# Kernel tuning notes

Measured on AMD Instinct MI355X. Metric: run time of the kernel, lower is better.

Reference implementation:

```python
import jax, jax.numpy as jnp
import numpy as np

B, P, ENC, DEC, ATT, EMB, V, CAPLEN = 128, 196, 2048, 512, 512, 300, 10000, 51


def setup_inputs() -> dict:
    key = jax.random.key(0)
    ks = jax.random.split(key, 20)
    s = 0.02
    lens = jax.random.randint(ks[2], (B, 1), 2, CAPLEN + 1)
    lens = lens.at[0, 0].set(CAPLEN)  # ensure max decode length == CAPLEN-1 (static T)
    return {
        'encoder_out': jax.random.normal(ks[0], (B, P, ENC), jnp.float32),
        'encoded_captions': jax.random.randint(ks[1], (B, CAPLEN), 0, V),
        'caption_lengths': lens,
        'W_enc_att': jax.random.normal(ks[3], (ATT, ENC)) * s,
        'b_enc_att': jnp.zeros((ATT,)),
        'W_dec_att': jax.random.normal(ks[4], (ATT, DEC)) * s,
        'b_dec_att': jnp.zeros((ATT,)),
        'w_full_att': jax.random.normal(ks[5], (ATT,)) * s,
        'b_full_att': jnp.zeros(()),
        'embedding': jax.random.uniform(ks[6], (V, EMB), minval=-0.1, maxval=0.1),
        'W_ih': jax.random.normal(ks[7], (4 * DEC, EMB + ENC)) * s,
        'b_ih': jnp.zeros((4 * DEC,)),
        'W_hh': jax.random.normal(ks[8], (4 * DEC, DEC)) * s,
        'b_hh': jnp.zeros((4 * DEC,)),
        'W_init_h': jax.random.normal(ks[9], (DEC, ENC)) * s,
        'b_init_h': jnp.zeros((DEC,)),
        'W_init_c': jax.random.normal(ks[10], (DEC, ENC)) * s,
        'b_init_c': jnp.zeros((DEC,)),
        'W_fbeta': jax.random.normal(ks[11], (ENC, DEC)) * s,
        'b_fbeta': jnp.zeros((ENC,)),
        'W_fc': jax.random.uniform(ks[12], (V, DEC), minval=-0.1, maxval=0.1),
        'b_fc': jnp.zeros((V,)),
    }


def reference(encoder_out, encoded_captions, caption_lengths,
              W_enc_att, b_enc_att, W_dec_att, b_dec_att, w_full_att, b_full_att,
              embedding, W_ih, b_ih, W_hh, b_hh,
              W_init_h, b_init_h, W_init_c, b_init_c,
              W_fbeta, b_fbeta, W_fc, b_fc):
    lens = caption_lengths[:, 0]
    sort_ind = jnp.argsort(-lens)                      # descending length sort
    lens_s = lens[sort_ind]
    enc = encoder_out[sort_ind]                        # [B,P,ENC]
    caps = encoded_captions[sort_ind]                  # [B,CAPLEN]
    emb = embedding[caps]                              # [B,CAPLEN,EMB]
    mean_enc = enc.mean(axis=1)
    h0 = mean_enc @ W_init_h.T + b_init_h
    c0 = mean_enc @ W_init_c.T + b_init_c
    att1 = enc @ W_enc_att.T + b_enc_att               # precomputed [B,P,ATT]
    decode_lengths = lens_s - 1
    T = caps.shape[1] - 1                              # static max decode length
    mask = jnp.arange(T)[:, None] < decode_lengths[None, :]   # [T,B]
    emb_t = jnp.transpose(emb[:, :T, :], (1, 0, 2))    # [T,B,EMB]

    def step(carry, xs):
        h, c = carry
        e_t, m_t = xs
        att2 = h @ W_dec_att.T + b_dec_att             # [B,ATT]
        score = jnp.einsum('bpa,a->bp', jax.nn.relu(att1 + att2[:, None, :]), w_full_att) + b_full_att
        alpha = jax.nn.softmax(score, axis=1)          # [B,P]
        awe = jnp.einsum('bp,bpe->be', alpha, enc)     # [B,ENC]
        gate = jax.nn.sigmoid(h @ W_fbeta.T + b_fbeta)
        awe = gate * awe
        x = jnp.concatenate([e_t, awe], axis=1)        # [B,EMB+ENC]
        gates = x @ W_ih.T + b_ih + h @ W_hh.T + b_hh
        i, f, g, o = jnp.split(gates, 4, axis=1)
        i, f, o = jax.nn.sigmoid(i), jax.nn.sigmoid(f), jax.nn.sigmoid(o)
        g = jnp.tanh(g)
        c_new = f * c + i * g
        h_new = o * jnp.tanh(c_new)
        m = m_t[:, None]
        # state only advances for still-active (length > t) rows
        h2 = jnp.where(m, h_new, h)
        c2 = jnp.where(m, c_new, c)
        preds = h_new @ W_fc.T + b_fc                  # dropout is identity in eval
        preds = jnp.where(m, preds, 0.0)
        alpha = jnp.where(m, alpha, 0.0)
        return (h2, c2), (preds, alpha)

    (_, _), (preds, alphas) = jax.lax.scan(step, (h0, c0), (emb_t, mask))
    predictions = jnp.transpose(preds, (1, 0, 2))      # [B,T,V]
    alphas = jnp.transpose(alphas, (1, 0, 2))          # [B,T,P]
    return predictions, caps, decode_lengths, alphas, sort_ind
```

## Files before the change

kernel.cpp:

```cpp
#include <hip/hip_runtime.h>
#include <math.h>

#define B 128
#define PP 196
#define ENC 2048
#define DEC 512
#define ATTD 512
#define EMB 300
#define VV 10000
#define CAPLEN 51
#define TT 50
#define KPAD 2880
#define NPPAD 10112

static const long long OFF_PRED = 0LL;
static const long long OFF_CAPS = 64000000LL;
static const long long OFF_DECL = 64006528LL;
static const long long OFF_ALPH = 64006656LL;
static const long long OFF_SORT = 65261056LL;

typedef unsigned short ushort_t;
typedef unsigned int uint_t;
typedef short bf8 __attribute__((ext_vector_type(8)));
typedef float f4 __attribute__((ext_vector_type(4)));

__device__ __forceinline__ float sigf(float x){ return 1.f/(1.f+expf(-x)); }
__device__ __forceinline__ float b2f(ushort_t u){
  union{uint_t i; float f;} v; v.i = ((uint_t)u)<<16; return v.f;
}
__device__ __forceinline__ ushort_t f2b(float f){
  union{float f; uint_t i;} v; v.f = f;
  uint_t r = v.i + 0x7fffu + ((v.i>>16)&1u);
  return (ushort_t)(r>>16);
}
__device__ __forceinline__ uint_t pack2(float lo, float hi){
  return (uint_t)f2b(lo) | ((uint_t)f2b(hi)<<16);
}
__device__ __forceinline__ float2 b2x2(uint_t u){
  union{uint_t i; float f;} a,b; a.i = u<<16; b.i = u & 0xffff0000u;
  return make_float2(a.f, b.f);
}

__device__ __forceinline__ void gemm128x64(
    const ushort_t* __restrict__ Ab, int lda, int m0,
    const ushort_t* __restrict__ Bb, int ldb, int n0,
    int Kbeg, int Kend, int mbound,
    ushort_t* As, ushort_t* Bs, int tid, f4 acc[4][2])
{
  const int r = tid>>2, cby = (tid&3)*8;
  const int w = tid>>6, l = tid&63;
  const int wm = w>>1, wn = w&1, lr = l&15, lk = (l>>4)*8;
  for (int k0=Kbeg; k0<Kend; k0+=32){
    uint4 qa0 = *(const uint4*)(Ab + (size_t)(m0+r)*lda    + k0 + cby);
    uint4 qa1 = *(const uint4*)(Ab + (size_t)(m0+64+r)*lda + k0 + cby);
    uint4 qb  = *(const uint4*)(Bb + (size_t)(n0+r)*ldb    + k0 + cby);
    __syncthreads();
    *(uint4*)(As + r*40      + cby) = qa0;
    *(uint4*)(As + (64+r)*40 + cby) = qa1;
    *(uint4*)(Bs + r*40      + cby) = qb;
    __syncthreads();
    bf8 b0 = *(const bf8*)(Bs + (wn*32+lr)*40    + lk);
    bf8 b1 = *(const bf8*)(Bs + (wn*32+16+lr)*40 + lk);
    #pragma unroll
    for (int fm=0; fm<4; fm++){
      if (wm*64 + fm*16 >= mbound) break;
      bf8 a = *(const bf8*)(As + (wm*64+fm*16+lr)*40 + lk);
      acc[fm][0] = __builtin_amdgcn_mfma_f32_16x16x32_bf16(a, b0, acc[fm][0], 0, 0, 0);
      acc[fm][1] = __builtin_amdgcn_mfma_f32_16x16x32_bf16(a, b1, acc[fm][1], 0, 0, 0);
    }
  }
}

__global__ __launch_bounds__(128) void k_prep(const int* __restrict__ cap_len,
    const int* __restrict__ enc_caps, float* __restrict__ out,
    int* __restrict__ sort_i, int* __restrict__ decl_i, int* __restrict__ caps_i,
    int* __restrict__ nact_d){
  __shared__ int lens[B];
  __shared__ int sind[B];
  __shared__ int s_dl[B];
  int t = threadIdx.x;
  lens[t] = cap_len[t];
  __syncthreads();
  int my = lens[t];
  int rank = 0;
  for (int j=0;j<B;j++){
    int lj = lens[j];
    if (lj > my || (lj == my && j < t)) rank++;
  }
  sind[rank] = t;
  __syncthreads();
  int src = sind[t];
  sort_i[t] = src;
  int dl = lens[src]-1;
  decl_i[t] = dl;
  s_dl[t] = dl;
  out[OFF_DECL+t] = (float)dl;
  out[OFF_SORT+t] = (float)src;
  for (int j=0;j<CAPLEN;j++){
    int v = enc_caps[src*CAPLEN+j];
    caps_i[t*CAPLEN+j] = v;
    out[OFF_CAPS + t*CAPLEN + j] = (float)v;
  }
  __syncthreads();
  if (t < TT){
    int cnt = 0;
    for (int b2=0;b2<B;b2++) cnt += (s_dl[b2] > t) ? 1 : 0;
    nact_d[t] = cnt;
  }
}

__global__ __launch_bounds__(256) void k_mean(const float* __restrict__ enc,
    const int* __restrict__ sort_i, float* __restrict__ meanb){
  int b = blockIdx.x;
  int e = blockIdx.y*256 + threadIdx.x;
  int sb = sort_i[b];
  const float* p0 = enc + (size_t)sb*PP*ENC + e;
  float s = 0.f;
  for (int p=0;p<PP;p++) s += p0[(size_t)p*ENC];
  meanb[b*ENC+e] = s * (1.0f/PP);
}

__global__ __launch_bounds__(256) void k_init(const float* __restrict__ meanb,
    const float* __restrict__ Wh, const float* __restrict__ bh,
    const float* __restrict__ Wc, const float* __restrict__ bc,
    float* __restrict__ h, float* __restrict__ c, ushort_t* __restrict__ xb_s){
  __shared__ float aT[64*132];
  __shared__ float wT[64*36];
  int tid = threadIdx.x;
  int n0 = blockIdx.x*32;
  const float* Wm  = blockIdx.y ? Wc : Wh;
  const float* bia = blockIdx.y ? bc : bh;
  float* dst = blockIdx.y ? c : h;
  int bt = tid&15, nt = tid>>4;
  float acc[8][2] = {};
  for (int k0=0;k0<ENC;k0+=64){
    for (int idx=tid; idx<64*128; idx+=256){
      int k=idx&63, m=idx>>6;
      aT[k*132+m] = meanb[m*ENC + k0+k];
    }
    for (int idx=tid; idx<64*32; idx+=256){
      int k=idx&63, n=idx>>6;
      wT[k*36+n] = Wm[(size_t)(n0+n)*ENC + k0+k];
    }
    __syncthreads();
    #pragma unroll 4
    for (int k=0;k<64;k++){
      float a[8], wv[2];
      *(float4*)&a[0] = *(const float4*)&aT[k*132+bt*8];
      *(float4*)&a[4] = *(const float4*)&aT[k*132+bt*8+4];
      *(float2*)&wv[0] = *(const float2*)&wT[k*36+nt*2];
      #pragma unroll
      for (int i=0;i<8;i++){ acc[i][0]+=a[i]*wv[0]; acc[i][1]+=a[i]*wv[1]; }
    }
    __syncthreads();
  }
  #pragma unroll
  for (int i=0;i<8;i++){
    int m = bt*8+i;
    #pragma unroll
    for (int j=0;j<2;j++){
      int n = n0+nt*2+j;
      float v = acc[i][j] + bia[n];
      dst[m*DEC+n] = v;
      if (blockIdx.y == 0) xb_s[(size_t)m*KPAD + n] = f2b(v);
    }
  }
}

__global__ __launch_bounds__(256) void k_wkb(const float* __restrict__ Whh,
    const float* __restrict__ Wih, uint_t* __restrict__ wkb_u){
  int n = blockIdx.x;
  uint_t* dst = wkb_u + (size_t)n*(KPAD/2);
  for (int u=threadIdx.x; u<KPAD/2; u+=256){
    int k = 2*u; float a, bvl;
    if (k < 512){ float2 v = *(const float2*)(Whh + (size_t)n*512 + k); a=v.x; bvl=v.y; }
    else if (k < 2860){ float2 v = *(const float2*)(Wih + (size_t)n*2348 + (k-512)); a=v.x; bvl=v.y; }
    else { a=0.f; bvl=0.f; }
    dst[u] = pack2(a, bvl);
  }
}
__global__ __launch_bounds__(256) void k_wcatb(const float* __restrict__ Wda,
    const float* __restrict__ Wfb, uint_t* __restrict__ wcat_u){
  int n = blockIdx.x;
  const float* src = (n < 512) ? (Wda + (size_t)n*512) : (Wfb + (size_t)(n-512)*512);
  uint_t* dst = wcat_u + (size_t)n*256;
  int u = threadIdx.x;
  float2 v = *(const float2*)(src + 2*u);
  dst[u] = pack2(v.x, v.y);
}
__global__ __launch_bounds__(256) void k_wfcb(const float* __restrict__ Wfc,
    uint_t* __restrict__ wfc_u){
  int n = blockIdx.x;
  uint_t* dst = wfc_u + (size_t)n*256;
  int u = threadIdx.x;
  if (n < VV){
    float2 v = *(const float2*)(Wfc + (size_t)n*512 + 2*u);
    dst[u] = pack2(v.x, v.y);
  } else dst[u] = 0u;
}
__global__ __launch_bounds__(256) void k_weab(const float* __restrict__ Wea,
    uint_t* __restrict__ wea_u){
  int n = blockIdx.x;
  uint_t* dst = wea_u + (size_t)n*1024;
  for (int u=threadIdx.x; u<1024; u+=256){
    float2 v = *(const float2*)(Wea + (size_t)n*2048 + 2*u);
    dst[u] = pack2(v.x, v.y);
  }
}
__global__ __launch_bounds__(160) void k_embb(const float* __restrict__ embedding,
    const int* __restrict__ caps_i, uint_t* __restrict__ embb_u){
  int b = blockIdx.x, t = blockIdx.y, tid = threadIdx.x;
  if (tid >= 150) return;
  int tok = caps_i[b*CAPLEN+t];
  float2 v = *(const float2*)(embedding + (size_t)tok*EMB + 2*tid);
  embb_u[((size_t)b*TT+t)*150 + tid] = pack2(v.x, v.y);
}
__global__ __launch_bounds__(256) void k_xpad(uint_t* __restrict__ xb_u){
  for (int u=threadIdx.x; u<1280; u+=256){
    int r = u/10, cu = u - r*10;
    xb_u[(size_t)r*(KPAD/2) + 1430 + cu] = 0u;
  }
}
__global__ __launch_bounds__(256) void k_encb(const float* __restrict__ enc,
    const int* __restrict__ sort_i, ushort_t* __restrict__ encb){
  int row = blockIdx.x;
  int b = row/PP, p = row - b*PP;
  int sb = sort_i[b];
  const float4* s4 = (const float4*)(enc + ((size_t)sb*PP+p)*ENC);
  uint4* d4 = (uint4*)(encb + (size_t)row*ENC);
  int tid = threadIdx.x;
  float4 f0 = s4[tid*2], f1 = s4[tid*2+1];
  uint4 q;
  q.x = pack2(f0.x,f0.y); q.y = pack2(f0.z,f0.w);
  q.z = pack2(f1.x,f1.y); q.w = pack2(f1.z,f1.w);
  d4[tid] = q;
}

__global__ __launch_bounds__(256) void k_zero(const int* __restrict__ decl_i,
    float* __restrict__ out){
  int blk = blockIdx.x;
  int b = blk/TT, t = blk - b*TT;
  if (t < decl_i[b]) return;
  float4 z = {0.f,0.f,0.f,0.f};
  float4* p = (float4*)(out + OFF_PRED + ((size_t)b*TT+t)*VV);
  for (int i=threadIdx.x; i<VV/4; i+=256) p[i] = z;
  size_t ao = (size_t)OFF_ALPH + ((size_t)b*TT+t)*PP;
  if (threadIdx.x < PP) out[ao + threadIdx.x] = 0.f;
}

__global__ __launch_bounds__(256) void k_att1g(const ushort_t* __restrict__ encb,
    const ushort_t* __restrict__ weab, const float* __restrict__ bea,
    ushort_t* __restrict__ attb){
  __shared__ ushort_t As[128*40];
  __shared__ ushort_t Bs[64*40];
  int tid = threadIdx.x;
  int m0 = blockIdx.x*128, n0 = blockIdx.y*64;
  f4 acc[4][2] = {};
  gemm128x64(encb, 2048, m0, weab, 2048, n0, 0, 2048, 128, As, Bs, tid, acc);
  int w = tid>>6, l = tid&63, wm = w>>1, wn = w&1;
  #pragma unroll
  for (int fm=0; fm<4; fm++)
    #pragma unroll
    for (int fn=0; fn<2; fn++)
      #pragma unroll
      for (int rr=0; rr<4; rr++){
        int m = m0 + wm*64 + fm*16 + (l>>4)*4 + rr;
        int n = n0 + wn*32 + fn*16 + (l&15);
        attb[(size_t)m*ATTD + n] = f2b(acc[fm][fn][rr] + bea[n]);
      }
}

__global__ __launch_bounds__(256) void k_att1_f32(const float* __restrict__ enc,
    const float* __restrict__ Wea, const float* __restrict__ bea,
    const int* __restrict__ sort_i, ushort_t* __restrict__ attb){
  __shared__ float aT[64*132];
  __shared__ float wT[64*68];
  int tid = threadIdx.x;
  int m0 = blockIdx.x*128;
  int n0 = blockIdx.y*64;
  int bt = tid&15, nt = tid>>4;
  float acc[8][4] = {};
  for (int k0=0;k0<ENC;k0+=64){
    for (int idx=tid; idx<64*128; idx+=256){
      int k=idx&63, m=idx>>6;
      int mg = m0+m;
      int b = mg/PP; int p = mg - b*PP;
      int sb = sort_i[b];
      aT[k*132+m] = enc[((size_t)sb*PP + p)*ENC + k0+k];
    }
    for (int idx=tid; idx<64*64; idx+=256){
      int k=idx&63, n=idx>>6;
      wT[k*68+n] = Wea[(size_t)(n0+n)*ENC + k0+k];
    }
    __syncthreads();
    #pragma unroll 4
    for (int k=0;k<64;k++){
      float a[8], wv[4];
      *(float4*)&a[0] = *(const float4*)&aT[k*132+bt*8];
      *(float4*)&a[4] = *(const float4*)&aT[k*132+bt*8+4];
      *(float4*)&wv[0] = *(const float4*)&wT[k*68+nt*4];
      #pragma unroll
      for (int i=0;i<8;i++)
        #pragma unroll
        for (int j=0;j<4;j++) acc[i][j] += a[i]*wv[j];
    }
    __syncthreads();
  }
  #pragma unroll
  for (int i=0;i<8;i++){
    int mg = m0+bt*8+i;
    #pragma unroll
    for (int j=0;j<4;j++){
      int n = n0+nt*4+j;
      attb[(size_t)mg*ATTD + n] = f2b(acc[i][j] + bea[n]);
    }
  }
}

__global__ __launch_bounds__(256) void k_hmats(const ushort_t* __restrict__ xb,
    const ushort_t* __restrict__ wcatb, const float* __restrict__ bda,
    const float* __restrict__ bfb, const int* __restrict__ nact_d,
    float* __restrict__ att2s, float* __restrict__ gate, int t){
  __shared__ ushort_t As[128*40];
  __shared__ ushort_t Bs[64*40];
  int tid = threadIdx.x;
  int n0 = blockIdx.x*64;
  int mb = nact_d[t];
  f4 acc[4][2] = {};
  gemm128x64(xb, KPAD, 0, wcatb, 512, n0, 0, 512, mb, As, Bs, tid, acc);
  int w = tid>>6, l = tid&63, wm = w>>1, wn = w&1;
  #pragma unroll
  for (int fm=0; fm<4; fm++)
    #pragma unroll
    for (int fn=0; fn<2; fn++)
      #pragma unroll
      for (int rr=0; rr<4; rr++){
        int m = wm*64 + fm*16 + (l>>4)*4 + rr;
        int n = n0 + wn*32 + fn*16 + (l&15);
        float v = acc[fm][fn][rr];
        if (n < 512) att2s[m*512+n] = v + bda[n];
        else         gate[m*2048 + (n-512)] = sigf(v + bfb[n-512]);
      }
}

template<bool FULLT>
__global__ __launch_bounds__(512) void k_score(const ushort_t* __restrict__ attb,
    const float* __restrict__ att2s, const float* __restrict__ wfa,
    const float* __restrict__ bfa, const int* __restrict__ decl_i,
    float* __restrict__ alb, float* __restrict__ out,
    uint_t* __restrict__ xb_u, const uint_t* __restrict__ embb_u,
    const float* __restrict__ embedding, const int* __restrict__ caps_i, int t){
  int b = blockIdx.x, tid = threadIdx.x;
  if (t >= decl_i[b]) return;
  __shared__ float s_a2[512], s_w[512], s_sc[200], s_red[8], s_red2[8];
  if (FULLT){
    if (tid < 150) xb_u[b*(KPAD/2) + 256 + tid] = embb_u[((size_t)b*TT+t)*150 + tid];
  } else {
    if (tid < 150){
      int tok = caps_i[b*CAPLEN+t];
      float2 e = *(const float2*)(embedding + (size_t)tok*EMB + 2*tid);
      xb_u[b*(KPAD/2) + 256 + tid] = pack2(e.x, e.y);
    }
  }
  s_a2[tid] = att2s[b*512+tid];
  s_w[tid]  = wfa[tid];
  __syncthreads();
  int wid = tid>>6, lane = tid&63;
  float b0 = bfa[0];
  for (int p=wid; p<PP; p+=8){
    uint4 q = ((const uint4*)(attb + ((size_t)b*PP + p)*ATTD))[lane];
    int j = lane*8;
    float2 x0=b2x2(q.x), x1=b2x2(q.y), x2=b2x2(q.z), x3=b2x2(q.w);
    float s = fmaxf(x0.x+s_a2[j+0],0.f)*s_w[j+0] + fmaxf(x0.y+s_a2[j+1],0.f)*s_w[j+1]
            + fmaxf(x1.x+s_a2[j+2],0.f)*s_w[j+2] + fmaxf(x1.y+s_a2[j+3],0.f)*s_w[j+3]
            + fmaxf(x2.x+s_a2[j+4],0.f)*s_w[j+4] + fmaxf(x2.y+s_a2[j+5],0.f)*s_w[j+5]
            + fmaxf(x3.x+s_a2[j+6],0.f)*s_w[j+6] + fmaxf(x3.y+s_a2[j+7],0.f)*s_w[j+7];
    #pragma unroll
    for (int off=32;off;off>>=1) s += __shfl_down(s,off);
    if (lane==0) s_sc[p] = s + b0;
  }
  __syncthreads();
  float sc = (tid<PP) ? s_sc[tid] : -1e30f;
  float mx = sc;
  #pragma unroll
  for (int off=32;off;off>>=1) mx = fmaxf(mx, __shfl_down(mx,off));
  if (lane==0) s_red[wid] = mx;
  __syncthreads();
  mx = s_red[0];
  #pragma unroll
  for (int i=1;i<8;i++) mx = fmaxf(mx, s_red[i]);
  float e = (tid<PP) ? expf(sc-mx) : 0.f;
  float sm = e;
  #pragma unroll
  for (int off=32;off;off>>=1) sm += __shfl_down(sm,off);
  if (lane==0) s_red2[wid] = sm;
  __syncthreads();
  float tot = 0.f;
  #pragma unroll
  for (int i=0;i<8;i++) tot += s_red2[i];
  float inv = 1.f/tot;
  if (tid<PP){
    float al = e*inv;
    alb[b*PP+tid] = al;
    out[(size_t)OFF_ALPH + ((size_t)b*TT+t)*PP + tid] = al;
  }
}

template<bool ENCB_>
__global__ __launch_bounds__(256) void k_awe(const ushort_t* __restrict__ encb,
    const float* __restrict__ enc, const int* __restrict__ sort_i,
    const float* __restrict__ alb, const float* __restrict__ gate,
    const int* __restrict__ decl_i, uint_t* __restrict__ xb_u, int t){
  int b = blockIdx.x, seg = blockIdx.y, tid = threadIdx.x;
  if (t >= decl_i[b]) return;
  __shared__ float s_al[PP];
  if (tid < PP) s_al[tid] = alb[b*PP+tid];
  __syncthreads();
  int ch = seg*512 + tid*2;
  float a0=0.f, a1=0.f;
  if (ENCB_){
    const uint_t* E = (const uint_t*)encb + (size_t)b*PP*(ENC/2) + (ch>>1);
    #pragma unroll 4
    for (int p=0;p<PP;p++){
      float2 u = b2x2(E[(size_t)p*(ENC/2)]);
      float al = s_al[p];
      a0 += al*u.x; a1 += al*u.y;
    }
  } else {
    const float2* E = (const float2*)(enc + (size_t)sort_i[b]*PP*ENC + ch);
    #pragma unroll 4
    for (int p=0;p<PP;p++){
      float2 u = E[(size_t)p*(ENC/2)];
      float al = s_al[p];
      a0 += al*u.x; a1 += al*u.y;
    }
  }
  float g0 = gate[b*ENC+ch], g1 = gate[b*ENC+ch+1];
  xb_u[b*(KPAD/2) + 406 + seg*256 + tid] = pack2(a0*g0, a1*g1);
}

__global__ __launch_bounds__(256) void k_b1g(const ushort_t* __restrict__ xb,
    const ushort_t* __restrict__ wkb, const int* __restrict__ nact_d,
    float* __restrict__ pbuf, int t){
  __shared__ ushort_t As[128*40];
  __shared__ ushort_t Bs[64*40];
  int tid = threadIdx.x;
  int n0 = blockIdx.x*64;
  int s  = blockIdx.y;
  int Kb = s*736, Ke = min(KPAD, Kb+736);
  int mb = nact_d[t];
  f4 acc[4][2] = {};
  gemm128x64(xb, KPAD, 0, wkb, KPAD, n0, Kb, Ke, mb, As, Bs, tid, acc);
  int w = tid>>6, l = tid&63, wm = w>>1, wn = w&1;
  #pragma unroll
  for (int fm=0; fm<4; fm++)
    #pragma unroll
    for (int fn=0; fn<2; fn++)
      #pragma unroll
      for (int rr=0; rr<4; rr++){
        int m = wm*64 + fm*16 + (l>>4)*4 + rr;
        int n = n0 + wn*32 + fn*16 + (l&15);
        pbuf[((size_t)s*B + m)*2048 + n] = acc[fm][fn][rr];
      }
}

__global__ __launch_bounds__(256) void k_b2(const float* __restrict__ pbuf,
    const float* __restrict__ b_ih, const float* __restrict__ b_hh,
    const int* __restrict__ decl_i, float* __restrict__ h, float* __restrict__ c,
    ushort_t* __restrict__ hnb, ushort_t* __restrict__ xb_s, int t){
  int b = blockIdx.x;
  int j = blockIdx.y*256 + threadIdx.x;
  float gi = b_ih[j]        + b_hh[j];
  float gf = b_ih[512+j]    + b_hh[512+j];
  float gg = b_ih[1024+j]   + b_hh[1024+j];
  float go = b_ih[1536+j]   + b_hh[1536+j];
  #pragma unroll
  for (int s=0;s<4;s++){
    const float* p = pbuf + ((size_t)s*B + b)*2048;
    gi += p[j]; gf += p[512+j]; gg += p[1024+j]; go += p[1536+j];
  }
  float hold = h[b*DEC+j];
  float cn = sigf(gf)*c[b*DEC+j] + sigf(gi)*tanhf(gg);
  float hn = sigf(go)*tanhf(cn);
  bool act = t < decl_i[b];
  if (act){ h[b*DEC+j] = hn; c[b*DEC+j] = cn; }
  hnb[b*DEC+j] = f2b(hn);
  xb_s[(size_t)b*KPAD + j] = f2b(act ? hn : hold);
}

__global__ __launch_bounds__(256) void k_predg(const ushort_t* __restrict__ hnb,
    const ushort_t* __restrict__ wfcb, const float* __restrict__ b_fc,
    const int* __restrict__ nact_d, float* __restrict__ out, int t){
  __shared__ ushort_t As[128*40];
  __shared__ ushort_t Bs[64*40];
  int tid = threadIdx.x;
  int n0 = blockIdx.x*64;
  int mb = nact_d[t];
  f4 acc[4][2] = {};
  gemm128x64(hnb, 512, 0, wfcb, 512, n0, 0, 512, mb, As, Bs, tid, acc);
  int w = tid>>6, l = tid&63, wm = w>>1, wn = w&1;
  #pragma unroll
  for (int fm=0; fm<4; fm++)
    #pragma unroll
    for (int fn=0; fn<2; fn++)
      #pragma unroll
      for (int rr=0; rr<4; rr++){
        int m = wm*64 + fm*16 + (l>>4)*4 + rr;
        int n = n0 + wn*32 + fn*16 + (l&15);
        if (m < mb && n < VV)
          out[OFF_PRED + ((size_t)m*TT + t)*VV + n] = acc[fm][fn][rr] + b_fc[n];
      }
}

extern "C" void kernel_launch(void* const* d_in, const int* in_sizes, int n_in,
                              void* d_out, int out_size, void* d_ws, size_t ws_size,
                              hipStream_t stream){
  const float* enc       = (const float*)d_in[0];
  const int*   caps_in   = (const int*)d_in[1];
  const int*   caplen    = (const int*)d_in[2];
  const float* W_enc_att = (const float*)d_in[3];
  const float* b_enc_att = (const float*)d_in[4];
  const float* W_dec_att = (const float*)d_in[5];
  const float* b_dec_att = (const float*)d_in[6];
  const float* w_full_att= (const float*)d_in[7];
  const float* b_full_att= (const float*)d_in[8];
  const float* embedding = (const float*)d_in[9];
  const float* W_ih      = (const float*)d_in[10];
  const float* b_ih      = (const float*)d_in[11];
  const float* W_hh      = (const float*)d_in[12];
  const float* b_hh      = (const float*)d_in[13];
  const float* W_init_h  = (const float*)d_in[14];
  const float* b_init_h  = (const float*)d_in[15];
  const float* W_init_c  = (const float*)d_in[16];
  const float* b_init_c  = (const float*)d_in[17];
  const float* W_fbeta   = (const float*)d_in[18];
  const float* b_fbeta   = (const float*)d_in[19];
  const float* W_fc      = (const float*)d_in[20];
  const float* b_fc      = (const float*)d_in[21];
  float* out = (float*)d_out;

  float* W = (float*)d_ws;
  size_t o = 0;
  auto A = [&](size_t n){ float* p = W + o; o += n; return p; };

  bool FULL = ws_size >= 168000000ull;

  float* h      = A(65536);
  float* c      = A(65536);
  float* att2s  = A(65536);
  float* gate   = A(262144);
  float* alb    = A(25088);
  float* meanb  = A(262144);
  float* pbuf   = A(1048576);
  ushort_t* xb   = (ushort_t*)A(184320);
  ushort_t* wkb  = (ushort_t*)A(2949120);
  ushort_t* wcatb= (ushort_t*)A(655360);
  ushort_t* wfcb = (ushort_t*)A(2588672);
  ushort_t* hnb  = (ushort_t*)A(32768);
  ushort_t* attb = (ushort_t*)A(6422528);
  int* ip = (int*)A(6848);
  int* sort_i = ip;
  int* decl_i = ip + 128;
  int* nact_d = ip + 256;
  int* caps_i = ip + 320;
  ushort_t* weab = nullptr;
  uint_t*   embb_u = nullptr;
  ushort_t* encb = nullptr;
  if (FULL){
    weab   = (ushort_t*)A(524288);
    embb_u = (uint_t*)A(960000);
    encb   = (ushort_t*)A(25690112);
  }
  uint_t* xb_u = (uint_t*)xb;

  k_prep<<<1,128,0,stream>>>(caplen, caps_in, out, sort_i, decl_i, caps_i, nact_d);
  k_mean<<<dim3(128,8),256,0,stream>>>(enc, sort_i, meanb);
  k_init<<<dim3(16,2),256,0,stream>>>(meanb, W_init_h, b_init_h, W_init_c, b_init_c, h, c, xb);
  k_wkb<<<2048,256,0,stream>>>(W_hh, W_ih, (uint_t*)wkb);
  k_wcatb<<<2560,256,0,stream>>>(W_dec_att, W_fbeta, (uint_t*)wcatb);
  k_wfcb<<<NPPAD,256,0,stream>>>(W_fc, (uint_t*)wfcb);
  k_xpad<<<1,256,0,stream>>>(xb_u);
  k_zero<<<6400,256,0,stream>>>(decl_i, out);
  if (FULL){
    k_weab<<<512,256,0,stream>>>(W_enc_att, (uint_t*)weab);
    k_embb<<<dim3(128,50),160,0,stream>>>(embedding, caps_i, embb_u);
    k_encb<<<25088,256,0,stream>>>(enc, sort_i, encb);
    k_att1g<<<dim3(196,8),256,0,stream>>>(encb, weab, b_enc_att, attb);
  } else {
    k_att1_f32<<<dim3(196,8),256,0,stream>>>(enc, W_enc_att, b_enc_att, sort_i, attb);
  }

  for (int t=0;t<TT;t++){
    k_hmats<<<40,256,0,stream>>>(xb, wcatb, b_dec_att, b_fbeta, nact_d, att2s, gate, t);
    if (FULL)
      k_score<true><<<128,512,0,stream>>>(attb, att2s, w_full_att, b_full_att, decl_i,
          alb, out, xb_u, embb_u, embedding, caps_i, t);
    else
      k_score<false><<<128,512,0,stream>>>(attb, att2s, w_full_att, b_full_att, decl_i,
          alb, out, xb_u, embb_u, embedding, caps_i, t);
    if (FULL)
      k_awe<true><<<dim3(128,4),256,0,stream>>>(encb, enc, sort_i, alb, gate, decl_i, xb_u, t);
    else
      k_awe<false><<<dim3(128,4),256,0,stream>>>(encb, enc, sort_i, alb, gate, decl_i, xb_u, t);
    k_b1g<<<dim3(32,4),256,0,stream>>>(xb, wkb, nact_d, pbuf, t);
    k_b2<<<dim3(128,2),256,0,stream>>>(pbuf, b_ih, b_hh, decl_i, h, c, hnb, xb, t);
    k_predg<<<158,256,0,stream>>>(hnb, wfcb, b_fc, nact_d, out, t);
  }
}
```

Measured before the change: 4.724 ms.

## Fuse score with attention-weighted sum, fuse LSTM GEMM with cell update, batch FC

Merges the attention softmax and the attention-weighted encoder sum into one kernel, and merges the LSTM gate GEMM with the cell update. This drops the split-K partial buffer and the per-step b2 kernel; interleaving the gate weight rows lets each block hold i/f/g/o for the same hidden units. The vocabulary projection moves out of the time loop into one batched launch over all steps, using stored hidden states. The shared GEMM helper also gains register prefetch of the next K tile. In exchange, the gate GEMM now runs the full K on only 32 blocks with no split-K, and the awe part runs on 128 blocks instead of 512.

```diff
diff --git a/kernel.cpp b/kernel.cpp
--- a/kernel.cpp
+++ b/kernel.cpp
@@ -50,23 +50,29 @@
   const int r = tid>>2, cby = (tid&3)*8;
   const int w = tid>>6, l = tid&63;
   const int wm = w>>1, wn = w&1, lr = l&15, lk = (l>>4)*8;
+  uint4 qa0 = *(const uint4*)(Ab + (size_t)(m0+r)*lda    + Kbeg + cby);
+  uint4 qa1 = *(const uint4*)(Ab + (size_t)(m0+64+r)*lda + Kbeg + cby);
+  uint4 qb  = *(const uint4*)(Bb + (size_t)(n0+r)*ldb    + Kbeg + cby);
   for (int k0=Kbeg; k0<Kend; k0+=32){
-    uint4 qa0 = *(const uint4*)(Ab + (size_t)(m0+r)*lda    + k0 + cby);
-    uint4 qa1 = *(const uint4*)(Ab + (size_t)(m0+64+r)*lda + k0 + cby);
-    uint4 qb  = *(const uint4*)(Bb + (size_t)(n0+r)*ldb    + k0 + cby);
     __syncthreads();
     *(uint4*)(As + r*40      + cby) = qa0;
     *(uint4*)(As + (64+r)*40 + cby) = qa1;
     *(uint4*)(Bs + r*40      + cby) = qb;
     __syncthreads();
+    if (k0+32 < Kend){
+      qa0 = *(const uint4*)(Ab + (size_t)(m0+r)*lda    + k0+32 + cby);
+      qa1 = *(const uint4*)(Ab + (size_t)(m0+64+r)*lda + k0+32 + cby);
+      qb  = *(const uint4*)(Bb + (size_t)(n0+r)*ldb    + k0+32 + cby);
+    }
     bf8 b0 = *(const bf8*)(Bs + (wn*32+lr)*40    + lk);
     bf8 b1 = *(const bf8*)(Bs + (wn*32+16+lr)*40 + lk);
     #pragma unroll
     for (int fm=0; fm<4; fm++){
-      if (wm*64 + fm*16 >= mbound) break;
-      bf8 a = *(const bf8*)(As + (wm*64+fm*16+lr)*40 + lk);
-      acc[fm][0] = __builtin_amdgcn_mfma_f32_16x16x32_bf16(a, b0, acc[fm][0], 0, 0, 0);
-      acc[fm][1] = __builtin_amdgcn_mfma_f32_16x16x32_bf16(a, b1, acc[fm][1], 0, 0, 0);
+      if (wm*64 + fm*16 < mbound){
+        bf8 a = *(const bf8*)(As + (wm*64+fm*16+lr)*40 + lk);
+        acc[fm][0] = __builtin_amdgcn_mfma_f32_16x16x32_bf16(a, b0, acc[fm][0], 0, 0, 0);
+        acc[fm][1] = __builtin_amdgcn_mfma_f32_16x16x32_bf16(a, b1, acc[fm][1], 0, 0, 0);
+      }
     }
   }
 }
@@ -170,11 +176,13 @@
 __global__ __launch_bounds__(256) void k_wkb(const float* __restrict__ Whh,
     const float* __restrict__ Wih, uint_t* __restrict__ wkb_u){
   int n = blockIdx.x;
+  int j = n>>2, g = n&3;
+  int rrow = g*512 + j;
   uint_t* dst = wkb_u + (size_t)n*(KPAD/2);
   for (int u=threadIdx.x; u<KPAD/2; u+=256){
     int k = 2*u; float a, bvl;
-    if (k < 512){ float2 v = *(const float2*)(Whh + (size_t)n*512 + k); a=v.x; bvl=v.y; }
-    else if (k < 2860){ float2 v = *(const float2*)(Wih + (size_t)n*2348 + (k-512)); a=v.x; bvl=v.y; }
+    if (k < 512){ float2 v = *(const float2*)(Whh + (size_t)rrow*512 + k); a=v.x; bvl=v.y; }
+    else if (k < 2860){ float2 v = *(const float2*)(Wih + (size_t)rrow*2348 + (k-512)); a=v.x; bvl=v.y; }
     else { a=0.f; bvl=0.f; }
     dst[u] = pack2(a, bvl);
   }
@@ -344,15 +352,17 @@
 }
 
 template<bool FULLT>
-__global__ __launch_bounds__(512) void k_score(const ushort_t* __restrict__ attb,
+__global__ __launch_bounds__(512) void k_score_awe(const ushort_t* __restrict__ attb,
     const float* __restrict__ att2s, const float* __restrict__ wfa,
     const float* __restrict__ bfa, const int* __restrict__ decl_i,
-    float* __restrict__ alb, float* __restrict__ out,
-    uint_t* __restrict__ xb_u, const uint_t* __restrict__ embb_u,
-    const float* __restrict__ embedding, const int* __restrict__ caps_i, int t){
+    const float* __restrict__ gate, const ushort_t* __restrict__ encb,
+    const float* __restrict__ enc, const int* __restrict__ sort_i,
+    float* __restrict__ out, uint_t* __restrict__ xb_u,
+    const uint_t* __restrict__ embb_u, const float* __restrict__ embedding,
+    const int* __restrict__ caps_i, int t){
   int b = blockIdx.x, tid = threadIdx.x;
   if (t >= decl_i[b]) return;
-  __shared__ float s_a2[512], s_w[512], s_sc[200], s_red[8], s_red2[8];
+  __shared__ float s_a2[512], s_w[512], s_sc[200], s_al[200], s_red[8], s_red2[8];
   if (FULLT){
     if (tid < 150) xb_u[b*(KPAD/2) + 256 + tid] = embb_u[((size_t)b*TT+t)*150 + tid];
   } else {
@@ -401,57 +411,58 @@
   float inv = 1.f/tot;
   if (tid<PP){
     float al = e*inv;
-    alb[b*PP+tid] = al;
+    s_al[tid] = al;
     out[(size_t)OFF_ALPH + ((size_t)b*TT+t)*PP + tid] = al;
   }
-}
-
-template<bool ENCB_>
-__global__ __launch_bounds__(256) void k_awe(const ushort_t* __restrict__ encb,
-    const float* __restrict__ enc, const int* __restrict__ sort_i,
-    const float* __restrict__ alb, const float* __restrict__ gate,
-    const int* __restrict__ decl_i, uint_t* __restrict__ xb_u, int t){
-  int b = blockIdx.x, seg = blockIdx.y, tid = threadIdx.x;
-  if (t >= decl_i[b]) return;
-  __shared__ float s_al[PP];
-  if (tid < PP) s_al[tid] = alb[b*PP+tid];
-  __syncthreads();
-  int ch = seg*512 + tid*2;
-  float a0=0.f, a1=0.f;
-  if (ENCB_){
-    const uint_t* E = (const uint_t*)encb + (size_t)b*PP*(ENC/2) + (ch>>1);
+  __syncthreads();
+  float a0=0.f,a1=0.f,a2=0.f,a3=0.f;
+  if (FULLT){
+    const uint2* E = (const uint2*)(encb + (size_t)b*PP*ENC) + tid;
     #pragma unroll 4
     for (int p=0;p<PP;p++){
-      float2 u = b2x2(E[(size_t)p*(ENC/2)]);
       float al = s_al[p];
-      a0 += al*u.x; a1 += al*u.y;
+      uint2 q = E[(size_t)p*(ENC/4)];
+      float2 u = b2x2(q.x), v = b2x2(q.y);
+      a0 += al*u.x; a1 += al*u.y; a2 += al*v.x; a3 += al*v.y;
     }
   } else {
-    const float2* E = (const float2*)(enc + (size_t)sort_i[b]*PP*ENC + ch);
+    const float4* E = (const float4*)(enc + (size_t)sort_i[b]*PP*ENC) + tid;
     #pragma unroll 4
     for (int p=0;p<PP;p++){
-      float2 u = E[(size_t)p*(ENC/2)];
       float al = s_al[p];
-      a0 += al*u.x; a1 += al*u.y;
-    }
-  }
-  float g0 = gate[b*ENC+ch], g1 = gate[b*ENC+ch+1];
-  xb_u[b*(KPAD/2) + 406 + seg*256 + tid] = pack2(a0*g0, a1*g1);
-}
-
-__global__ __launch_bounds__(256) void k_b1g(const ushort_t* __restrict__ xb,
-    const ushort_t* __restrict__ wkb, const int* __restrict__ nact_d,
-    float* __restrict__ pbuf, int t){
+      float4 q = E[(size_t)p*(ENC/4)];
+      a0 += al*q.x; a1 += al*q.y; a2 += al*q.z; a3 += al*q.w;
+    }
+  }
+  float4 g = *(const float4*)(gate + b*2048 + tid*4);
+  xb_u[b*(KPAD/2) + 406 + tid*2]     = pack2(a0*g.x, a1*g.y);
+  xb_u[b*(KPAD/2) + 406 + tid*2 + 1] = pack2(a2*g.z, a3*g.w);
+}
+
+__global__ __launch_bounds__(256) void k_b1gf(const ushort_t* __restrict__ xb,
+    const ushort_t* __restrict__ wkbi, const float* __restrict__ b_ih,
+    const float* __restrict__ b_hh, const int* __restrict__ decl_i,
+    const int* __restrict__ nact_d, float* __restrict__ c,
+    ushort_t* __restrict__ hnball, ushort_t* __restrict__ xb_s, int t){
   __shared__ ushort_t As[128*40];
   __shared__ ushort_t Bs[64*40];
+  __shared__ float sacc[128*68];
+  __shared__ float sbias[64];
+  __shared__ int s_dl[128];
   int tid = threadIdx.x;
   int n0 = blockIdx.x*64;
-  int s  = blockIdx.y;
-  int Kb = s*736, Ke = min(KPAD, Kb+736);
+  int j0 = n0>>2;
   int mb = nact_d[t];
+  if (tid < 64){
+    int n = n0 + tid;
+    int j = n>>2, g = n&3;
+    sbias[tid] = b_ih[g*512+j] + b_hh[g*512+j];
+  }
+  if (tid < 128) s_dl[tid] = decl_i[tid];
   f4 acc[4][2] = {};
-  gemm128x64(xb, KPAD, 0, wkb, KPAD, n0, Kb, Ke, mb, As, Bs, tid, acc);
+  gemm128x64(xb, KPAD, 0, wkbi, KPAD, n0, 0, KPAD, mb, As, Bs, tid, acc);
   int w = tid>>6, l = tid&63, wm = w>>1, wn = w&1;
+  __syncthreads();
   #pragma unroll
   for (int fm=0; fm<4; fm++)
     #pragma unroll
@@ -459,45 +470,40 @@
       #pragma unroll
       for (int rr=0; rr<4; rr++){
         int m = wm*64 + fm*16 + (l>>4)*4 + rr;
-        int n = n0 + wn*32 + fn*16 + (l&15);
-        pbuf[((size_t)s*B + m)*2048 + n] = acc[fm][fn][rr];
+        int n = wn*32 + fn*16 + (l&15);
+        sacc[m*68+n] = acc[fm][fn][rr];
       }
-}
-
-__global__ __launch_bounds__(256) void k_b2(const float* __restrict__ pbuf,
-    const float* __restrict__ b_ih, const float* __restrict__ b_hh,
-    const int* __restrict__ decl_i, float* __restrict__ h, float* __restrict__ c,
-    ushort_t* __restrict__ hnb, ushort_t* __restrict__ xb_s, int t){
-  int b = blockIdx.x;
-  int j = blockIdx.y*256 + threadIdx.x;
-  float gi = b_ih[j]        + b_hh[j];
-  float gf = b_ih[512+j]    + b_hh[512+j];
-  float gg = b_ih[1024+j]   + b_hh[1024+j];
-  float go = b_ih[1536+j]   + b_hh[1536+j];
-  #pragma unroll
-  for (int s=0;s<4;s++){
-    const float* p = pbuf + ((size_t)s*B + b)*2048;
-    gi += p[j]; gf += p[512+j]; gg += p[1024+j]; go += p[1536+j];
-  }
-  float hold = h[b*DEC+j];
-  float cn = sigf(gf)*c[b*DEC+j] + sigf(gi)*tanhf(gg);
-  float hn = sigf(go)*tanhf(cn);
-  bool act = t < decl_i[b];
-  if (act){ h[b*DEC+j] = hn; c[b*DEC+j] = cn; }
-  hnb[b*DEC+j] = f2b(hn);
-  xb_s[(size_t)b*KPAD + j] = f2b(act ? hn : hold);
-}
-
-__global__ __launch_bounds__(256) void k_predg(const ushort_t* __restrict__ hnb,
+  __syncthreads();
+  #pragma unroll
+  for (int q=0; q<8; q++){
+    int idx = q*256 + tid;
+    int m = idx>>4, u = idx&15;
+    int j = j0 + u;
+    float gi = sacc[m*68 + u*4+0] + sbias[u*4+0];
+    float gf = sacc[m*68 + u*4+1] + sbias[u*4+1];
+    float gg = sacc[m*68 + u*4+2] + sbias[u*4+2];
+    float go = sacc[m*68 + u*4+3] + sbias[u*4+3];
+    float cn = sigf(gf)*c[m*512+j] + sigf(gi)*tanhf(gg);
+    float hn = sigf(go)*tanhf(cn);
+    hnball[((size_t)t*B + m)*512 + j] = f2b(hn);
+    if (t < s_dl[m]){
+      c[m*512+j] = cn;
+      xb_s[(size_t)m*KPAD + j] = f2b(hn);
+    }
+  }
+}
+
+__global__ __launch_bounds__(256) void k_predall(const ushort_t* __restrict__ hnball,
     const ushort_t* __restrict__ wfcb, const float* __restrict__ b_fc,
-    const int* __restrict__ nact_d, float* __restrict__ out, int t){
+    const int* __restrict__ nact_d, float* __restrict__ out){
   __shared__ ushort_t As[128*40];
   __shared__ ushort_t Bs[64*40];
   int tid = threadIdx.x;
+  int t = blockIdx.y;
   int n0 = blockIdx.x*64;
   int mb = nact_d[t];
   f4 acc[4][2] = {};
-  gemm128x64(hnb, 512, 0, wfcb, 512, n0, 0, 512, mb, As, Bs, tid, acc);
+  gemm128x64(hnball + (size_t)t*B*512, 512, 0, wfcb, 512, n0, 0, 512, mb, As, Bs, tid, acc);
   int w = tid>>6, l = tid&63, wm = w>>1, wn = w&1;
   #pragma unroll
   for (int fm=0; fm<4; fm++)
@@ -543,21 +549,19 @@
   size_t o = 0;
   auto A = [&](size_t n){ float* p = W + o; o += n; return p; };
 
-  bool FULL = ws_size >= 168000000ull;
+  bool FULL = ws_size >= 172000000ull;
 
   float* h      = A(65536);
   float* c      = A(65536);
   float* att2s  = A(65536);
   float* gate   = A(262144);
-  float* alb    = A(25088);
   float* meanb  = A(262144);
-  float* pbuf   = A(1048576);
-  ushort_t* xb   = (ushort_t*)A(184320);
-  ushort_t* wkb  = (ushort_t*)A(2949120);
-  ushort_t* wcatb= (ushort_t*)A(655360);
-  ushort_t* wfcb = (ushort_t*)A(2588672);
-  ushort_t* hnb  = (ushort_t*)A(32768);
-  ushort_t* attb = (ushort_t*)A(6422528);
+  ushort_t* xb    = (ushort_t*)A(184320);
+  ushort_t* wkb   = (ushort_t*)A(2949120);
+  ushort_t* wcatb = (ushort_t*)A(655360);
+  ushort_t* wfcb  = (ushort_t*)A(2588672);
+  ushort_t* hnball= (ushort_t*)A(1638400);
+  ushort_t* attb  = (ushort_t*)A(6422528);
   int* ip = (int*)A(6848);
   int* sort_i = ip;
   int* decl_i = ip + 128;
@@ -593,17 +597,12 @@
   for (int t=0;t<TT;t++){
     k_hmats<<<40,256,0,stream>>>(xb, wcatb, b_dec_att, b_fbeta, nact_d, att2s, gate, t);
     if (FULL)
-      k_score<true><<<128,512,0,stream>>>(attb, att2s, w_full_att, b_full_att, decl_i,
-          alb, out, xb_u, embb_u, embedding, caps_i, t);
+      k_score_awe<true><<<128,512,0,stream>>>(attb, att2s, w_full_att, b_full_att, decl_i,
+          gate, encb, enc, sort_i, out, xb_u, embb_u, embedding, caps_i, t);
     else
-      k_score<false><<<128,512,0,stream>>>(attb, att2s, w_full_att, b_full_att, decl_i,
-          alb, out, xb_u, embb_u, embedding, caps_i, t);
-    if (FULL)
-      k_awe<true><<<dim3(128,4),256,0,stream>>>(encb, enc, sort_i, alb, gate, decl_i, xb_u, t);
-    else
-      k_awe<false><<<dim3(128,4),256,0,stream>>>(encb, enc, sort_i, alb, gate, decl_i, xb_u, t);
-    k_b1g<<<dim3(32,4),256,0,stream>>>(xb, wkb, nact_d, pbuf, t);
-    k_b2<<<dim3(128,2),256,0,stream>>>(pbuf, b_ih, b_hh, decl_i, h, c, hnb, xb, t);
-    k_predg<<<158,256,0,stream>>>(hnb, wfcb, b_fc, nact_d, out, t);
-  }
-}
+      k_score_awe<false><<<128,512,0,stream>>>(attb, att2s, w_full_att, b_full_att, decl_i,
+          gate, encb, enc, sort_i, out, xb_u, embb_u, embedding, caps_i, t);
+    k_b1gf<<<32,256,0,stream>>>(xb, wkb, b_ih, b_hh, decl_i, nact_d, c, hnball, xb, t);
+  }
+  k_predall<<<dim3(158,TT),256,0,stream>>>(hnball, wfcb, b_fc, nact_d, out);
+}
```

New measurement: 5.269 ms. 11.5% more time.
